# Kernel optimization log

Measured on AMD Instinct MI355X. Metric: run time of the kernel, lower is better.

Reference implementation:

```python
import jax, jax.numpy as jnp
import numpy as np

B, S, D, V = 512, 4096, 128, 6
SPARSITY = 0.1
PAD_IDX = 5


def setup_inputs() -> dict:
    key = jax.random.key(0)
    ks = jax.random.split(key, 16)
    n = lambda k, shape: (jax.random.normal(k, shape, jnp.float32) * 0.02)
    emb = n(ks[0], (V, D)).at[PAD_IDX].set(0.0)  # padding_idx=5 row zeroed
    # importance_network: D -> D/2 -> D/4 -> 1
    W1 = n(ks[1], (D, D // 2)); b1 = jnp.zeros((D // 2,), jnp.float32)
    W2 = n(ks[2], (D // 2, D // 4)); b2 = jnp.zeros((D // 4,), jnp.float32)
    W3 = n(ks[3], (D // 4, 1)); b3 = jnp.zeros((1,), jnp.float32)
    # attention_approximator: D -> D/2 -> D (dropout = identity in eval)
    A1 = n(ks[4], (D, D // 2)); a1 = jnp.zeros((D // 2,), jnp.float32)
    A2 = n(ks[5], (D // 2, D)); a2 = jnp.zeros((D,), jnp.float32)
    # classifier: D -> D/2 -> 1 -> sigmoid
    C1 = n(ks[6], (D, D // 2)); c1 = jnp.zeros((D // 2,), jnp.float32)
    C2 = n(ks[7], (D // 2, 1)); c2 = jnp.zeros((1,), jnp.float32)
    x = jax.random.randint(ks[8], (B, S), 0, V, dtype=jnp.int64 if jax.config.jax_enable_x64 else jnp.int32)
    return dict(x=x, emb=emb, W1=W1, b1=b1, W2=W2, b2=b2, W3=W3, b3=b3,
                A1=A1, a1=a1, A2=A2, a2=a2, C1=C1, c1=c1, C2=C2, c2=c2)


def reference(x, emb, W1, b1, W2, b2, W3, b3, A1, a1, A2, a2, C1, c1, C2, c2):
    batch, seq = x.shape
    k = max(1, int(seq * SPARSITY))  # 409
    e = emb[x]  # [B,S,D] embedding lookup
    # importance MLP + sigmoid -> learned scores [B,S]
    h = jax.nn.relu(e @ W1 + b1)
    h = jax.nn.relu(h @ W2 + b2)
    final_scores = jax.nn.sigmoid((h @ W3 + b3)[..., 0])  # [B,S]
    # topk select + gather embeddings (irregular access)
    top_vals, top_idx = jax.lax.top_k(final_scores, k)  # [B,k]
    sel = jnp.take_along_axis(e, top_idx[..., None], axis=1)  # [B,k,D]
    # attention approximator MLP
    attended = jax.nn.relu(sel @ A1 + a1) @ A2 + a2  # [B,k,D]
    pooled = attended.mean(axis=1)  # [B,D]
    # classifier
    pred = jax.nn.sigmoid((jax.nn.relu(pooled @ C1 + c1) @ C2 + c2))[..., 0]  # [B]
    return pred, top_idx, final_scores
```

## Files before the change

### kernel.cpp

```cpp
#include <hip/hip_runtime.h>
#include <hip/hip_bf16.h>
#include <math.h>

#define BB 512
#define SS 4096
#define DD 128
#define VV 6
#define KK 409


__global__ __launch_bounds__(256) void precompute_kernel(
    const float* __restrict__ emb,
    const float* __restrict__ W1, const float* __restrict__ b1,
    const float* __restrict__ W2, const float* __restrict__ b2,
    const float* __restrict__ W3, const float* __restrict__ b3,
    const float* __restrict__ A1, const float* __restrict__ a1,
    const float* __restrict__ A2, const float* __restrict__ a2,
    float* __restrict__ ws)
{
    __shared__ float sW1[DD * 64];
    __shared__ float sA1[DD * 64];
    __shared__ float sW2[64 * 32];
    __shared__ float sA2[64 * DD];
    __shared__ float sE[VV * DD];
    __shared__ float sW3[32];
    __shared__ float sb1[64], sb2[32], sa1[64], sa2[DD];
    __shared__ float sh1[VV * 64], sg[VV * 64], sh2[VV * 32];
    __shared__ float sb3;

    const int tid = threadIdx.x;

    {
        const float* srcs[9] = { W1, A1, W2, A2, emb, b1, b2, a1, a2 };
        float*       dsts[9] = { sW1, sA1, sW2, sA2, sE, sb1, sb2, sa1, sa2 };
        const int    ns[9]   = { 8192, 8192, 2048, 8192, VV*DD, 64, 32, 64, DD };
        for (int a = 0; a < 9; ++a) {
            const float4* s4 = (const float4*)srcs[a];
            float4* d4 = (float4*)dsts[a];
            const int n4 = ns[a] >> 2;
            for (int i = tid; i < n4; i += 256) d4[i] = s4[i];
        }
        if (tid < 32) sW3[tid] = W3[tid];
        if (tid == 0) sb3 = b3[0];
    }
    __syncthreads();

    for (int u = tid; u < 768; u += 256) {
        const int isH = (u < 384) ? 1 : 0;
        const int v = isH ? u : (u - 384);
        const int t = v >> 6, o = v & 63;
        const float* wcol = isH ? sW1 : sA1;
        float acc = isH ? sb1[o] : sa1[o];
        const float* ev = &sE[t * DD];
        #pragma unroll 8
        for (int d = 0; d < DD; ++d) acc += ev[d] * wcol[d * 64 + o];
        acc = fmaxf(acc, 0.f);
        if (isH) sh1[v] = acc; else sg[v] = acc;
    }
    __syncthreads();

    for (int u = tid; u < VV * 32; u += 256) {
        const int t = u >> 5, o = u & 31;
        float acc = sb2[o];
        #pragma unroll 8
        for (int j = 0; j < 64; ++j) acc += sh1[t * 64 + j] * sW2[j * 32 + o];
        sh2[u] = fmaxf(acc, 0.f);
    }
    __syncthreads();

    for (int u = tid; u < 6 + VV * DD; u += 256) {
        if (u < 6) {
            float s = sb3;
            #pragma unroll
            for (int j = 0; j < 32; ++j) s += sh2[u * 32 + j] * sW3[j];
            ws[u] = 1.f / (1.f + expf(-s));
        } else {
            const int v = u - 6;
            const int t = v >> 7, o = v & 127;
            float acc = sa2[o];
            #pragma unroll 8
            for (int j = 0; j < 64; ++j) acc += sg[t * 64 + j] * sA2[j * DD + o];
            ws[16 + v] = acc;
        }
    }
}

__global__ __launch_bounds__(256) void row_kernel(
    const int* __restrict__ x,
    const float* __restrict__ ws,
    const float* __restrict__ C1, const float* __restrict__ c1,
    const float* __restrict__ C2, const float* __restrict__ c2,
    float* __restrict__ pred, float* __restrict__ topk, float* __restrict__ fsc)
{
    __shared__ float sc[VV];
    __shared__ float att_s[VV*DD];
    __shared__ int   waveTot[4*VV];
    __shared__ float pooled[DD];
    __shared__ float hcls[64];

    const int tid  = threadIdx.x;
    const int b    = blockIdx.x;
    const int lane = tid & 63;
    const int w    = tid >> 6;

    if (tid < VV) sc[tid] = ws[tid];
    for (int i = tid; i < VV*DD; i += 256) att_s[i] = ws[16 + i];
    __syncthreads();

    const int base = b*SS + tid*16;
    int vals[16];
    const int4* xp = (const int4*)(x + base);
    #pragma unroll
    for (int q = 0; q < 4; ++q) {
        int4 v = xp[q];
        vals[q*4+0]=v.x; vals[q*4+1]=v.y; vals[q*4+2]=v.z; vals[q*4+3]=v.w;
    }
    float4* op = (float4*)(fsc + base);
    #pragma unroll
    for (int q = 0; q < 4; ++q) {
        float4 o;
        o.x = sc[vals[q*4+0]];
        o.y = sc[vals[q*4+1]];
        o.z = sc[vals[q*4+2]];
        o.w = sc[vals[q*4+3]];
        op[q] = o;
    }
    int lc[VV];
    #pragma unroll
    for (int t = 0; t < VV; ++t) {
        int c = 0;
        #pragma unroll
        for (int i = 0; i < 16; ++i) c += (vals[i] == t) ? 1 : 0;
        lc[t] = c;
    }

    int excl[VV];
    #pragma unroll
    for (int t = 0; t < VV; ++t) {
        int v = lc[t];
        #pragma unroll
        for (int off = 1; off < 64; off <<= 1) {
            int u = __shfl_up(v, off, 64);
            if (lane >= off) v += u;
        }
        excl[t] = v - lc[t];
        if (lane == 63) waveTot[w*VV + t] = v;
    }
    __syncthreads();

    int rowTot[VV], woff[VV];
    #pragma unroll
    for (int t = 0; t < VV; ++t) {
        int a0 = waveTot[0*VV+t], a1v = waveTot[1*VV+t];
        int a2v = waveTot[2*VV+t], a3v = waveTot[3*VV+t];
        rowTot[t] = a0 + a1v + a2v + a3v;
        int wo = 0;
        if (w > 0) wo += a0;
        if (w > 1) wo += a1v;
        if (w > 2) wo += a2v;
        woff[t] = wo;
    }

    float s_reg[VV];
    #pragma unroll
    for (int t = 0; t < VV; ++t) s_reg[t] = sc[t];
    int pri[VV];
    #pragma unroll
    for (int t = 0; t < VV; ++t) {
        int p = 0;
        #pragma unroll
        for (int u = 0; u < VV; ++u)
            p += ((s_reg[u] > s_reg[t]) || ((s_reg[u] == s_reg[t]) && (u < t))) ? 1 : 0;
        pri[t] = p;
    }
    int start[VV], m[VV];
    #pragma unroll
    for (int t = 0; t < VV; ++t) {
        int cb = 0;
        #pragma unroll
        for (int u = 0; u < VV; ++u)
            cb += (pri[u] < pri[t]) ? rowTot[u] : 0;
        int mm = KK - cb;
        mm = (mm < 0) ? 0 : mm;
        mm = (mm > rowTot[t]) ? rowTot[t] : mm;
        m[t] = mm;
        start[t] = cb + woff[t] + excl[t];
    }

    #pragma unroll
    for (int t = 0; t < VV; ++t) {
        int pos = start[t];
        #pragma unroll
        for (int i = 0; i < 16; ++i) {
            if (vals[i] == t) {
                if (pos < KK) topk[b*KK + pos] = (float)(tid*16 + i);
                pos++;
            }
        }
    }

    if (tid < DD) {
        float acc = 0.f;
        #pragma unroll
        for (int t = 0; t < VV; ++t) acc += (float)m[t] * att_s[t*DD + tid];
        pooled[tid] = acc * (1.0f / (float)KK);
    }
    __syncthreads();
    if (tid < 64) {
        float acc = c1[tid];
        for (int d = 0; d < DD; ++d) acc += pooled[d] * C1[d*64 + tid];
        hcls[tid] = fmaxf(acc, 0.f);
    }
    __syncthreads();
    if (tid == 0) {
        float s = c2[0];
        for (int j = 0; j < 64; ++j) s += hcls[j] * C2[j];
        pred[b] = 1.f / (1.f + expf(-s));
    }
}

extern "C" void kernel_launch(void* const* d_in, const int* in_sizes, int n_in,
                              void* d_out, int out_size, void* d_ws, size_t ws_size,
                              hipStream_t stream)
{
    (void)in_sizes; (void)n_in; (void)out_size; (void)ws_size;
    const int*   x   = (const int*)d_in[0];
    const float* emb = (const float*)d_in[1];
    const float* W1  = (const float*)d_in[2];
    const float* b1  = (const float*)d_in[3];
    const float* W2  = (const float*)d_in[4];
    const float* b2  = (const float*)d_in[5];
    const float* W3  = (const float*)d_in[6];
    const float* b3  = (const float*)d_in[7];
    const float* A1  = (const float*)d_in[8];
    const float* a1  = (const float*)d_in[9];
    const float* A2  = (const float*)d_in[10];
    const float* a2  = (const float*)d_in[11];
    const float* C1  = (const float*)d_in[12];
    const float* c1  = (const float*)d_in[13];
    const float* C2  = (const float*)d_in[14];
    const float* c2  = (const float*)d_in[15];

    float* out  = (float*)d_out;
    float* pred = out;
    float* topk = out + BB;
    float* fsc  = out + BB + BB*KK;
    float* ws   = (float*)d_ws;

    precompute_kernel<<<1, 256, 0, stream>>>(emb, W1, b1, W2, b2, W3, b3,
                                             A1, a1, A2, a2, ws);
    row_kernel<<<BB, 256, 0, stream>>>(x, ws, C1, c1, C2, c2, pred, topk, fsc);
}
```

Baseline: 116.7 us.

## Fuse per-token-value precompute into row kernel, recomputing MLP tables per block

Removes the single-block precompute kernel and its serial dependency by having every one of the 512 row blocks recompute the 6-entry score and attention tables itself. A single shared buffer is reused for W1, A1 and A2 to keep LDS usage low, and the x load is issued early to overlap with the weight staging. This trades one launch and a grid-wide serialization for redundant weight loads (about 100KB per block, mostly L2 hits) and extra per-block compute.

```diff
diff --git a/kernel.cpp b/kernel.cpp
--- a/kernel.cpp
+++ b/kernel.cpp
@@ -8,33 +8,49 @@
 #define VV 6
 #define KK 409
 
-
-__global__ __launch_bounds__(256) void precompute_kernel(
+__global__ __launch_bounds__(256) void fused_kernel(
+    const int* __restrict__ x,
     const float* __restrict__ emb,
     const float* __restrict__ W1, const float* __restrict__ b1,
     const float* __restrict__ W2, const float* __restrict__ b2,
     const float* __restrict__ W3, const float* __restrict__ b3,
     const float* __restrict__ A1, const float* __restrict__ a1,
     const float* __restrict__ A2, const float* __restrict__ a2,
-    float* __restrict__ ws)
+    const float* __restrict__ C1, const float* __restrict__ c1,
+    const float* __restrict__ C2, const float* __restrict__ c2,
+    float* __restrict__ pred, float* __restrict__ topk, float* __restrict__ fsc)
 {
-    __shared__ float sW1[DD * 64];
-    __shared__ float sA1[DD * 64];
+    __shared__ float sBuf[DD * 64];
     __shared__ float sW2[64 * 32];
-    __shared__ float sA2[64 * DD];
     __shared__ float sE[VV * DD];
     __shared__ float sW3[32];
     __shared__ float sb1[64], sb2[32], sa1[64], sa2[DD];
-    __shared__ float sh1[VV * 64], sg[VV * 64], sh2[VV * 32];
     __shared__ float sb3;
-
-    const int tid = threadIdx.x;
-
-    {
-        const float* srcs[9] = { W1, A1, W2, A2, emb, b1, b2, a1, a2 };
-        float*       dsts[9] = { sW1, sA1, sW2, sA2, sE, sb1, sb2, sa1, sa2 };
-        const int    ns[9]   = { 8192, 8192, 2048, 8192, VV*DD, 64, 32, 64, DD };
-        for (int a = 0; a < 9; ++a) {
+    __shared__ float sh1[VV * 64];
+    __shared__ float sh2[VV * 32];
+    __shared__ float sc[VV];
+    __shared__ float att_s[VV * DD];
+    __shared__ int   waveTot[4 * VV];
+    __shared__ float pooled[DD];
+    __shared__ float hcls[64];
+
+    const int tid  = threadIdx.x;
+    const int b    = blockIdx.x;
+    const int lane = tid & 63;
+    const int w    = tid >> 6;
+
+    const int base = b * SS + tid * 16;
+    const int4* xp = (const int4*)(x + base);
+    int4 xv[4];
+    #pragma unroll
+    for (int q = 0; q < 4; ++q) xv[q] = xp[q];
+
+    {
+        const float* srcs[7] = { W1, W2, emb, b1, b2, a1, a2 };
+        float*       dsts[7] = { sBuf, sW2, sE, sb1, sb2, sa1, sa2 };
+        const int    ns[7]   = { 8192, 2048, VV * DD, 64, 32, 64, DD };
+        #pragma unroll
+        for (int a = 0; a < 7; ++a) {
             const float4* s4 = (const float4*)srcs[a];
             float4* d4 = (float4*)dsts[a];
             const int n4 = ns[a] >> 2;
@@ -45,20 +61,21 @@
     }
     __syncthreads();
 
-    for (int u = tid; u < 768; u += 256) {
-        const int isH = (u < 384) ? 1 : 0;
-        const int v = isH ? u : (u - 384);
-        const int t = v >> 6, o = v & 63;
-        const float* wcol = isH ? sW1 : sA1;
-        float acc = isH ? sb1[o] : sa1[o];
+    for (int u = tid; u < VV * 64; u += 256) {
+        const int t = u >> 6, o = u & 63;
+        float acc = sb1[o];
         const float* ev = &sE[t * DD];
         #pragma unroll 8
-        for (int d = 0; d < DD; ++d) acc += ev[d] * wcol[d * 64 + o];
-        acc = fmaxf(acc, 0.f);
-        if (isH) sh1[v] = acc; else sg[v] = acc;
-    }
-    __syncthreads();
-
+        for (int d = 0; d < DD; ++d) acc += ev[d] * sBuf[d * 64 + o];
+        sh1[u] = fmaxf(acc, 0.f);
+    }
+    __syncthreads();
+
+    {
+        const float4* s4 = (const float4*)A1;
+        float4* d4 = (float4*)sBuf;
+        for (int i = tid; i < 2048; i += 256) d4[i] = s4[i];
+    }
     for (int u = tid; u < VV * 32; u += 256) {
         const int t = u >> 5, o = u & 31;
         float acc = sb2[o];
@@ -68,62 +85,44 @@
     }
     __syncthreads();
 
-    for (int u = tid; u < 6 + VV * DD; u += 256) {
-        if (u < 6) {
-            float s = sb3;
-            #pragma unroll
-            for (int j = 0; j < 32; ++j) s += sh2[u * 32 + j] * sW3[j];
-            ws[u] = 1.f / (1.f + expf(-s));
-        } else {
-            const int v = u - 6;
-            const int t = v >> 7, o = v & 127;
-            float acc = sa2[o];
-            #pragma unroll 8
-            for (int j = 0; j < 64; ++j) acc += sg[t * 64 + j] * sA2[j * DD + o];
-            ws[16 + v] = acc;
-        }
-    }
-}
-
-__global__ __launch_bounds__(256) void row_kernel(
-    const int* __restrict__ x,
-    const float* __restrict__ ws,
-    const float* __restrict__ C1, const float* __restrict__ c1,
-    const float* __restrict__ C2, const float* __restrict__ c2,
-    float* __restrict__ pred, float* __restrict__ topk, float* __restrict__ fsc)
-{
-    __shared__ float sc[VV];
-    __shared__ float att_s[VV*DD];
-    __shared__ int   waveTot[4*VV];
-    __shared__ float pooled[DD];
-    __shared__ float hcls[64];
-
-    const int tid  = threadIdx.x;
-    const int b    = blockIdx.x;
-    const int lane = tid & 63;
-    const int w    = tid >> 6;
-
-    if (tid < VV) sc[tid] = ws[tid];
-    for (int i = tid; i < VV*DD; i += 256) att_s[i] = ws[16 + i];
-    __syncthreads();
-
-    const int base = b*SS + tid*16;
+    if (tid < VV) {
+        float s = sb3;
+        #pragma unroll
+        for (int j = 0; j < 32; ++j) s += sh2[tid * 32 + j] * sW3[j];
+        sc[tid] = 1.f / (1.f + expf(-s));
+    }
+    for (int u = tid; u < VV * 64; u += 256) {
+        const int t = u >> 6, o = u & 63;
+        float acc = sa1[o];
+        const float* ev = &sE[t * DD];
+        #pragma unroll 8
+        for (int d = 0; d < DD; ++d) acc += ev[d] * sBuf[d * 64 + o];
+        sh1[u] = fmaxf(acc, 0.f);
+    }
+    __syncthreads();
+
+    {
+        const float4* s4 = (const float4*)A2;
+        float4* d4 = (float4*)sBuf;
+        for (int i = tid; i < 2048; i += 256) d4[i] = s4[i];
+    }
     int vals[16];
-    const int4* xp = (const int4*)(x + base);
     #pragma unroll
     for (int q = 0; q < 4; ++q) {
-        int4 v = xp[q];
-        vals[q*4+0]=v.x; vals[q*4+1]=v.y; vals[q*4+2]=v.z; vals[q*4+3]=v.w;
-    }
-    float4* op = (float4*)(fsc + base);
-    #pragma unroll
-    for (int q = 0; q < 4; ++q) {
-        float4 o;
-        o.x = sc[vals[q*4+0]];
-        o.y = sc[vals[q*4+1]];
-        o.z = sc[vals[q*4+2]];
-        o.w = sc[vals[q*4+3]];
-        op[q] = o;
+        vals[q*4+0] = xv[q].x; vals[q*4+1] = xv[q].y;
+        vals[q*4+2] = xv[q].z; vals[q*4+3] = xv[q].w;
+    }
+    {
+        float4* op = (float4*)(fsc + base);
+        #pragma unroll
+        for (int q = 0; q < 4; ++q) {
+            float4 o;
+            o.x = sc[vals[q*4+0]];
+            o.y = sc[vals[q*4+1]];
+            o.z = sc[vals[q*4+2]];
+            o.w = sc[vals[q*4+3]];
+            op[q] = o;
+        }
     }
     int lc[VV];
     #pragma unroll
@@ -133,7 +132,15 @@
         for (int i = 0; i < 16; ++i) c += (vals[i] == t) ? 1 : 0;
         lc[t] = c;
     }
-
+    __syncthreads();
+
+    for (int u = tid; u < VV * DD; u += 256) {
+        const int t = u >> 7, o = u & 127;
+        float acc = sa2[o];
+        #pragma unroll 8
+        for (int j = 0; j < 64; ++j) acc += sh1[t * 64 + j] * sBuf[j * DD + o];
+        att_s[u] = acc;
+    }
     int excl[VV];
     #pragma unroll
     for (int t = 0; t < VV; ++t) {
@@ -144,7 +151,7 @@
             if (lane >= off) v += u;
         }
         excl[t] = v - lc[t];
-        if (lane == 63) waveTot[w*VV + t] = v;
+        if (lane == 63) waveTot[w * VV + t] = v;
     }
     __syncthreads();
 
@@ -160,7 +167,6 @@
         if (w > 2) wo += a2v;
         woff[t] = wo;
     }
-
     float s_reg[VV];
     #pragma unroll
     for (int t = 0; t < VV; ++t) s_reg[t] = sc[t];
@@ -193,7 +199,7 @@
         #pragma unroll
         for (int i = 0; i < 16; ++i) {
             if (vals[i] == t) {
-                if (pos < KK) topk[b*KK + pos] = (float)(tid*16 + i);
+                if (pos < KK) topk[b * KK + pos] = (float)(tid * 16 + i);
                 pos++;
             }
         }
@@ -202,18 +208,20 @@
     if (tid < DD) {
         float acc = 0.f;
         #pragma unroll
-        for (int t = 0; t < VV; ++t) acc += (float)m[t] * att_s[t*DD + tid];
+        for (int t = 0; t < VV; ++t) acc += (float)m[t] * att_s[t * DD + tid];
         pooled[tid] = acc * (1.0f / (float)KK);
     }
     __syncthreads();
     if (tid < 64) {
         float acc = c1[tid];
-        for (int d = 0; d < DD; ++d) acc += pooled[d] * C1[d*64 + tid];
+        #pragma unroll 8
+        for (int d = 0; d < DD; ++d) acc += pooled[d] * C1[d * 64 + tid];
         hcls[tid] = fmaxf(acc, 0.f);
     }
     __syncthreads();
     if (tid == 0) {
         float s = c2[0];
+        #pragma unroll 8
         for (int j = 0; j < 64; ++j) s += hcls[j] * C2[j];
         pred[b] = 1.f / (1.f + expf(-s));
     }
@@ -223,7 +231,7 @@
                               void* d_out, int out_size, void* d_ws, size_t ws_size,
                               hipStream_t stream)
 {
-    (void)in_sizes; (void)n_in; (void)out_size; (void)ws_size;
+    (void)in_sizes; (void)n_in; (void)out_size; (void)d_ws; (void)ws_size;
     const int*   x   = (const int*)d_in[0];
     const float* emb = (const float*)d_in[1];
     const float* W1  = (const float*)d_in[2];
@@ -245,9 +253,8 @@
     float* pred = out;
     float* topk = out + BB;
     float* fsc  = out + BB + BB*KK;
-    float* ws   = (float*)d_ws;
-
-    precompute_kernel<<<1, 256, 0, stream>>>(emb, W1, b1, W2, b2, W3, b3,
-                                             A1, a1, A2, a2, ws);
-    row_kernel<<<BB, 256, 0, stream>>>(x, ws, C1, c1, C2, c2, pred, topk, fsc);
+
+    fused_kernel<<<BB, 256, 0, stream>>>(x, emb, W1, b1, W2, b2, W3, b3,
+                                         A1, a1, A2, a2, C1, c1, C2, c2,
+                                         pred, topk, fsc);
 }
```

After: 115.9 us. Within noise of the previous version (-0.6%).
